# Kernel optimization log

Hardware: AMD Instinct MI355X
Metric: run time of the kernel (lower is better)

## Reference

```python
import jax, jax.numpy as jnp
import numpy as np

B, S, D = 4, 2048, 2048
D_INNER = max(128, D // 2)  # 1024, torch default d_inner
FO = 2                      # filter_order
K = 3                       # kernel_size
KS = 3                      # short_kernel_size


def setup_inputs() -> dict:
    key = jax.random.key(0)
    ks = jax.random.split(key, 6)
    return {
        "x": jax.random.normal(ks[0], (B, S, D), jnp.float32),
        # depthwise short conv: weight (D, KS), bias (D,)
        "short_w": jax.random.normal(ks[1], (D, KS), jnp.float32) / np.float32(np.sqrt(KS)),
        "short_b": jnp.zeros((D,), jnp.float32),
        # filter MLP proj: Linear(D -> FO*D_INNER)
        "proj_w": jax.random.normal(ks[2], (D, FO * D_INNER), jnp.float32) / np.float32(np.sqrt(D)),
        "proj_b": jnp.zeros((FO * D_INNER,), jnp.float32),
        # filter MLP output: Linear(D_INNER -> K), SHARED across filter orders
        "filt_w": jax.random.normal(ks[3], (D_INNER, K), jnp.float32) / np.float32(np.sqrt(D_INNER)),
        "filt_b": jnp.zeros((K,), jnp.float32),
        # output projection Linear(D -> D)
        "out_w": jax.random.normal(ks[4], (D, D), jnp.float32) / np.float32(np.sqrt(D)),
        "out_b": jnp.zeros((D,), jnp.float32),
    }


def reference(x, short_w, short_b, proj_w, proj_b, filt_w, filt_b, out_w, out_b):
    b, s, d = x.shape
    v = x  # v captured BEFORE short-conv residual, as in the torch code

    # --- causal depthwise short conv (pad k-1 on left, truncate to s) ---
    xp = jnp.pad(x, ((0, 0), (KS - 1, 0), (0, 0)))
    x_short = short_b
    for j in range(KS):  # tiny fixed kernel loop
        x_short = x_short + xp[:, j:j + s, :] * short_w[:, j]
    x = x + x_short

    # --- filter function: Linear -> GELU -> (shared) Linear -> tanh ---
    h = jax.nn.gelu(x @ proj_w + proj_b, approximate=False)         # (b, s, FO*D_INNER)
    h = h.reshape(b, s, FO, D_INNER)
    filt = jnp.tanh(jnp.einsum('bsfi,ik->bsfk', h, filt_w) + filt_b)  # (b, s, FO, K)

    # --- gated depthwise conv: kernel = mean over seq, shared across channels;
    # sum over filter orders commutes with the (linear) conv, so fold it in ---
    w = filt.mean(axis=1).sum(axis=1)                                # (b, K)
    xp2 = jnp.pad(x, ((0, 0), (K - 1, 0), (0, 0)))
    conv = jnp.zeros_like(x)
    for j in range(K):
        conv = conv + xp2[:, j:j + s, :] * w[:, j][:, None, None]

    # --- gate with v, GELU, output projection ---
    y = jax.nn.gelu(conv * v, approximate=False)
    return y @ out_w + out_b
```

## Files before the change

### kernel.cpp

```cpp
#include <hip/hip_runtime.h>
#include <hip/hip_bf16.h>
#include <math.h>

typedef unsigned short u16;
typedef __attribute__((ext_vector_type(4))) unsigned short u16x4;
typedef __attribute__((ext_vector_type(8))) unsigned short u16x8;
typedef __attribute__((ext_vector_type(8))) short s16x8;
typedef __attribute__((ext_vector_type(4))) float f32x4;

#define B_  4
#define S_  2048
#define D_  2048
#define DI_ 1024
#define MROWS (B_ * S_)
#define KDIM  D_
#define NDIM  D_
#define STRIP 16

__device__ __forceinline__ float b2f(u16 u) {
    union { unsigned i; float f; } v; v.i = ((unsigned)u) << 16; return v.f;
}
__device__ __forceinline__ u16 f2b(float f) {
    unsigned u = __float_as_uint(f);
    unsigned r = (u + 0x7FFFu + ((u >> 16) & 1u)) >> 16;
    return (u16)r;
}
__device__ __forceinline__ float gelu_exact(float x) {
    return 0.5f * x * (1.0f + erff(x * 0.70710678118654752f));
}

#define GLOAD_LDS16(gp, lp)                                                    \
    __builtin_amdgcn_global_load_lds(                                          \
        (const __attribute__((address_space(1))) void*)(gp),                   \
        (__attribute__((address_space(3))) void*)(lp), 16, 0, 0)

__global__ void prep_k(const float* __restrict__ in0, u16* __restrict__ out0,
                       const float* __restrict__ in1, u16* __restrict__ out1,
                       int nt,
                       const float* __restrict__ x, const float* __restrict__ sw,
                       const float* __restrict__ sb, u16* __restrict__ xs,
                       float* __restrict__ wacc, float* __restrict__ t_g,
                       unsigned* __restrict__ cnt) {
    const int bid = blockIdx.x;
    const int tid = threadIdx.x;
    const int tblocks = nt << 12;
    if (bid < tblocks) {
        __shared__ float tile[32][33];
        const float* in = (bid >> 12) ? in1 : in0;
        u16* out = (bid >> 12) ? out1 : out0;
        const int t2 = bid & 4095;
        const int bx = (t2 & 63) << 5, by = (t2 >> 6) << 5;
        const int tx = tid & 31, ty = tid >> 5;
        for (int i = 0; i < 32; i += 8)
            tile[ty + i][tx] = in[(size_t)(by + ty + i) * D_ + bx + tx];
        __syncthreads();
        for (int i = 0; i < 32; i += 8)
            out[(size_t)(bx + ty + i) * D_ + by + tx] = f2b(tile[tx][ty + i]);
        return;
    }
    const int f = bid - tblocks;
    {
        int z = f * 256 + tid;
        if (z < 12) wacc[z] = 0.0f;
        if (z == 12) *cnt = 0u;
        if (z < MROWS * 6) t_g[z] = 0.0f;
    }
    const int c = (f & 1) * 1024 + tid * 4;
    const int r0 = (f >> 1) * STRIP;
    const int t0 = r0 & (S_ - 1);

    float tap[12];
    #pragma unroll
    for (int q = 0; q < 3; ++q)
        ((f32x4*)tap)[q] = *(const f32x4*)(sw + (size_t)c * 3 + q * 4);
    f32x4 sbv = *(const f32x4*)(sb + c);

    const float* base = x + (size_t)r0 * D_ + c;
    f32x4 m2, m1;
    if (t0 == 0) { m2 = (f32x4)(0.0f); m1 = (f32x4)(0.0f); }
    else { m2 = *(const f32x4*)(base - 2 * D_); m1 = *(const f32x4*)(base - D_); }

    u16* op = xs + (size_t)r0 * D_ + c;
    #pragma unroll
    for (int rr = 0; rr < STRIP; ++rr) {
        f32x4 cur = *(const f32x4*)(base + (size_t)rr * D_);
        u16x4 outv;
        #pragma unroll
        for (int e = 0; e < 4; ++e) {
            float v = cur[e] + sbv[e]
                    + tap[e * 3 + 0] * m2[e]
                    + tap[e * 3 + 1] * m1[e]
                    + tap[e * 3 + 2] * cur[e];
            outv[e] = f2b(v);
        }
        *(u16x4*)(op + (size_t)rr * D_) = outv;
        m2 = m1; m1 = cur;
    }
}

__global__ void transpose_k(const float* __restrict__ in, u16* __restrict__ out) {
    __shared__ float tile[32][33];
    int bx = blockIdx.x * 32, by = blockIdx.y * 32;
    int tx = threadIdx.x & 31, ty = threadIdx.x >> 5;
    for (int i = 0; i < 32; i += 8)
        tile[ty + i][tx] = in[(size_t)(by + ty + i) * D_ + bx + tx];
    __syncthreads();
    for (int i = 0; i < 32; i += 8)
        out[(size_t)(bx + ty + i) * D_ + by + tx] = f2b(tile[tx][ty + i]);
}

#define STG_A(REG, KOFF) do { const u16* _g = gA + (KOFF);                     \
    GLOAD_LDS16(_g, &As[REG][ldsW0]);                                          \
    GLOAD_LDS16(_g + (size_t)128 * KDIM, &As[REG][ldsW1]); } while (0)
#define STG_B(REG, KOFF) do { const u16* _g = gB + (KOFF);                     \
    GLOAD_LDS16(_g, &Bs[REG][ldsW0]);                                          \
    GLOAD_LDS16(_g + (size_t)128 * KDIM, &Bs[REG][ldsW1]); } while (0)
#define LD_AH(R_) do {                                                         \
    aH[0] = *(const s16x8*)&As[R_][aoffR[4]];                                  \
    aH[1] = *(const s16x8*)&As[R_][aoffR[5]];                                  \
    aH[2] = *(const s16x8*)&As[R_][aoffR[6]];                                  \
    aH[3] = *(const s16x8*)&As[R_][aoffR[7]]; } while (0)
#define LD_ALBC(S_, R_) do {                                                   \
    aL[S_][0] = *(const s16x8*)&As[R_][aoffR[0]];                              \
    aL[S_][1] = *(const s16x8*)&As[R_][aoffR[1]];                              \
    aL[S_][2] = *(const s16x8*)&As[R_][aoffR[2]];                              \
    aL[S_][3] = *(const s16x8*)&As[R_][aoffR[3]];                              \
    bC[S_][0] = *(const s16x8*)&Bs[R_][boffR[0]];                              \
    bC[S_][1] = *(const s16x8*)&Bs[R_][boffR[1]];                              \
    bC[S_][2] = *(const s16x8*)&Bs[R_][boffR[2]];                              \
    bC[S_][3] = *(const s16x8*)&Bs[R_][boffR[3]]; } while (0)
#define MFMA_LO(S_) do { __builtin_amdgcn_s_setprio(1);                        \
    _Pragma("unroll")                                                          \
    for (int i_ = 0; i_ < 4; ++i_) {                                           \
        _Pragma("unroll")                                                      \
        for (int j_ = 0; j_ < 4; ++j_)                                         \
            acc[i_][j_] = __builtin_amdgcn_mfma_f32_16x16x32_bf16(             \
                aL[S_][i_], bC[S_][j_], acc[i_][j_], 0, 0, 0);                 \
    }                                                                          \
    __builtin_amdgcn_s_setprio(0); } while (0)
#define MFMA_HI(S_) do { __builtin_amdgcn_s_setprio(1);                        \
    _Pragma("unroll")                                                          \
    for (int i_ = 0; i_ < 4; ++i_) {                                           \
        _Pragma("unroll")                                                      \
        for (int j_ = 0; j_ < 4; ++j_)                                         \
            acc[4 + i_][j_] = __builtin_amdgcn_mfma_f32_16x16x32_bf16(         \
                aH[i_], bC[S_][j_], acc[4 + i_][j_], 0, 0, 0);                 \
    }                                                                          \
    __builtin_amdgcn_s_setprio(0); } while (0)
#define BARR() __builtin_amdgcn_s_barrier()
#define VM8() asm volatile("s_waitcnt vmcnt(8)" ::: "memory")
#define VM4() asm volatile("s_waitcnt vmcnt(4)" ::: "memory")
#define VM0() asm volatile("s_waitcnt vmcnt(0)" ::: "memory")
#define VMNOP()

#define TILE(T_, R_, RN_, CS_, NS_, DOSTG_, GATE_, DOPF_) do {                 \
    BARR();                                                                    \
    if (DOSTG_) { STG_A((((R_) + 3) & 3), ((T_) + 3) * 32);                    \
                  STG_B((((R_) + 3) & 3), ((T_) + 3) * 32); }                  \
    LD_AH(R_);                                                                 \
    MFMA_LO(CS_);                                                              \
    GATE_;                                                                     \
    BARR();                                                                    \
    if (DOPF_) { LD_ALBC(NS_, RN_); }                                          \
    MFMA_HI(CS_);                                                              \
} while (0)

#define GEMM_CORE_OL(APTR, BPTR)                                               \
    __shared__ u16 As[4][8192];                                                \
    __shared__ u16 Bs[4][8192];                                                \
    const int tid  = threadIdx.x;                                              \
    const int wid  = tid >> 6;                                                 \
    const int lane = tid & 63;                                                 \
    const int wr   = wid >> 2;                                                 \
    const int wc   = wid & 3;                                                  \
    const int lid_ = (blockIdx.y << 3) | blockIdx.x;                           \
    const int wsw_ = ((lid_ & 7) << 5) | (lid_ >> 3);         \
    const int row0 = (wsw_ >> 3) << 8;                                         \
    const int col0 = (wsw_ & 7) << 8;                                          \
    const int rowS    = tid >> 2;                                              \
    const int colOffS = (((tid & 3) ^ ((rowS >> 1) & 3)) << 3);                \
    const u16* gA = (APTR) + (size_t)(row0 + rowS) * KDIM + colOffS;           \
    const u16* gB = (BPTR) + (size_t)(col0 + rowS) * KDIM + colOffS;           \
    const int ldsW0 = wid * 512;                                               \
    const int ldsW1 = 4096 + wid * 512;                                        \
    int aoffR[8], boffR[4];                                                    \
    _Pragma("unroll")                                                          \
    for (int i = 0; i < 8; ++i) {                                              \
        int row  = (wr << 7) + (i << 4) + (lane & 15);                         \
        int slot = (lane >> 4) ^ ((row >> 1) & 3);                             \
        aoffR[i] = row * 32 + slot * 8;                                        \
    }                                                                          \
    _Pragma("unroll")                                                          \
    for (int j = 0; j < 4; ++j) {                                              \
        int row  = (wc << 6) + (j << 4) + (lane & 15);                         \
        int slot = (lane >> 4) ^ ((row >> 1) & 3);                             \
        boffR[j] = row * 32 + slot * 8;                                        \
    }                                                                          \
    f32x4 acc[8][4];                                                           \
    _Pragma("unroll")                                                          \
    for (int i = 0; i < 8; ++i)                                                \
        _Pragma("unroll")                                                      \
        for (int j = 0; j < 4; ++j) acc[i][j] = (f32x4)(0.0f);                 \
    s16x8 aL[2][4], bC[2][4], aH[4];                                           \
    STG_A(0, 0);  STG_B(0, 0);                                                 \
    STG_A(1, 32); STG_B(1, 32);                                                \
    STG_A(2, 64); STG_B(2, 64);                                                \
    VM8();                                                                     \
    BARR();                                                                    \
    LD_ALBC(0, 0);                                                             \
    _Pragma("unroll 1")                                                        \
    for (int t = 0; t < 15; ++t) {                                             \
        const int T4 = t * 4;                                                  \
        TILE(T4 + 0, 0, 1, 0, 1, 1, VM8(), 1);                                 \
        TILE(T4 + 1, 1, 2, 1, 0, 1, VM8(), 1);                                 \
        TILE(T4 + 2, 2, 3, 0, 1, 1, VM8(), 1);                                 \
        TILE(T4 + 3, 3, 0, 1, 0, 1, VM8(), 1);                                 \
    }                                                                          \
    TILE(60, 0, 1, 0, 1, 1, VM8(), 1);                                         \
    TILE(61, 1, 2, 1, 0, 0, VM4(), 1);                                         \
    TILE(62, 2, 3, 0, 1, 0, VM0(), 1);                                         \
    TILE(63, 3, 0, 1, 0, 0, VMNOP(), 0);

__global__ __launch_bounds__(512, 2)
void gemm_f8(const u16* __restrict__ A, const u16* __restrict__ BT,
             const float* __restrict__ bias,
             const float* __restrict__ fw, float* __restrict__ t_g,
             const float* __restrict__ fb, unsigned* __restrict__ cnt,
             float* __restrict__ wacc) {
    GEMM_CORE_OL(A, BT)

    __shared__ float t_lds[768];
    __shared__ unsigned done_s;
    __syncthreads();
    for (int z = tid; z < 768; z += 512) t_lds[z] = 0.0f;
    __syncthreads();

    const int colt0 = (wc << 6) + (lane & 15);
    float fwv[4][3], bsv[4];
    const int ibase = (col0 & (DI_ - 1)) + colt0;
    #pragma unroll
    for (int j = 0; j < 4; ++j) {
        int ifilt = ibase + j * 16;
        fwv[j][0] = fw[ifilt * 3 + 0];
        fwv[j][1] = fw[ifilt * 3 + 1];
        fwv[j][2] = fw[ifilt * 3 + 2];
        bsv[j] = bias[col0 + colt0 + j * 16];
    }
    #pragma unroll
    for (int i = 0; i < 8; ++i) {
        #pragma unroll
        for (int r = 0; r < 4; ++r) {
            float s0 = 0.f, s1 = 0.f, s2 = 0.f;
            #pragma unroll
            for (int j = 0; j < 4; ++j) {
                float hv = gelu_exact(acc[i][j][r] + bsv[j]);
                s0 += hv * fwv[j][0];
                s1 += hv * fwv[j][1];
                s2 += hv * fwv[j][2];
            }
            #pragma unroll
            for (int m = 1; m < 16; m <<= 1) {
                s0 += __shfl_xor(s0, m, 16);
                s1 += __shfl_xor(s1, m, 16);
                s2 += __shfl_xor(s2, m, 16);
            }
            if ((lane & 15) == 0) {
                int trow = (wr << 7) + ((lane >> 4) << 2) + (i << 4) + r;
                atomicAdd(&t_lds[trow * 3 + 0], s0);
                atomicAdd(&t_lds[trow * 3 + 1], s1);
                atomicAdd(&t_lds[trow * 3 + 2], s2);
            }
        }
    }
    __syncthreads();
    const int f3 = (col0 >= DI_) ? 3 : 0;
    for (int z = tid; z < 768; z += 512) {
        int rr = z / 3, k = z - rr * 3;
        atomicAdd(&t_g[(size_t)(row0 + rr) * 6 + f3 + k], t_lds[z]);
    }

    __threadfence();
    __syncthreads();
    if (tid == 0) done_s = atomicAdd(cnt, 1u);
    __syncthreads();
    if (done_s == 255u) {
        const float fb0 = fb[0], fb1 = fb[1], fb2 = fb[2];
        for (int b = 0; b < B_; ++b) {
            float s0 = 0.f, s1 = 0.f, s2 = 0.f;
            for (int p = tid; p < 2 * S_; p += 512) {
                int row = (b << 11) + (p >> 1);
                int fo  = p & 1;
                const float* tp = t_g + (size_t)row * 6 + fo * 3;
                float a0 = __hip_atomic_load(tp + 0, __ATOMIC_RELAXED,
                                             __HIP_MEMORY_SCOPE_AGENT);
                float a1 = __hip_atomic_load(tp + 1, __ATOMIC_RELAXED,
                                             __HIP_MEMORY_SCOPE_AGENT);
                float a2 = __hip_atomic_load(tp + 2, __ATOMIC_RELAXED,
                                             __HIP_MEMORY_SCOPE_AGENT);
                s0 += tanhf(a0 + fb0);
                s1 += tanhf(a1 + fb1);
                s2 += tanhf(a2 + fb2);
            }
            #pragma unroll
            for (int m = 1; m < 64; m <<= 1) {
                s0 += __shfl_xor(s0, m, 64);
                s1 += __shfl_xor(s1, m, 64);
                s2 += __shfl_xor(s2, m, 64);
            }
            __syncthreads();
            if (lane == 0) {
                t_lds[wid * 3 + 0] = s0;
                t_lds[wid * 3 + 1] = s1;
                t_lds[wid * 3 + 2] = s2;
            }
            __syncthreads();
            if (tid < 3) {
                float s = 0.f;
                #pragma unroll
                for (int w = 0; w < 8; ++w) s += t_lds[w * 3 + tid];
                wacc[b * 3 + tid] = s;
            }
        }
    }
}

__global__ __launch_bounds__(256, 2)
void gemm2_tlp(const u16* __restrict__ A, const u16* __restrict__ BT,
               const float* __restrict__ bias, float* __restrict__ C) {
    __shared__ u16 As[2][8192];
    __shared__ u16 Bs[2][4096];

    const int tid  = threadIdx.x;
    const int wid  = tid >> 6;
    const int lane = tid & 63;
    const int wr   = wid >> 1;
    const int wc   = wid & 1;
    const int lid  = (blockIdx.y << 4) | blockIdx.x;
    const int wsw  = ((lid & 7) << 6) | (lid >> 3);
    const int row0 = (wsw >> 4) << 8;
    const int col0 = (wsw & 15) << 7;

    const int srow = tid >> 2;
    const int cSw  = (((tid & 3) ^ ((srow >> 1) & 3)) << 3);
    const u16* gA0 = A  + (size_t)(row0 + srow) * KDIM + cSw;
    const u16* gB0 = BT + (size_t)(col0 + srow) * KDIM + cSw;
    const int ldsW = wid * 512;

#define STG2(R_, KOFF) do {                                                    \
    const u16* _ga = gA0 + (KOFF);                                             \
    const u16* _gb = gB0 + (KOFF);                                             \
    GLOAD_LDS16(_ga,                      &As[R_][ldsW]);                      \
    GLOAD_LDS16(_ga + (size_t)64 * KDIM,  &As[R_][2048 + ldsW]);               \
    GLOAD_LDS16(_ga + (size_t)128 * KDIM, &As[R_][4096 + ldsW]);               \
    GLOAD_LDS16(_ga + (size_t)192 * KDIM, &As[R_][6144 + ldsW]);               \
    GLOAD_LDS16(_gb,                      &Bs[R_][ldsW]);                      \
    GLOAD_LDS16(_gb + (size_t)64 * KDIM,  &Bs[R_][2048 + ldsW]);               \
} while (0)

    int aoffR[8], boffR[4];
    #pragma unroll
    for (int i = 0; i < 8; ++i) {
        int row  = (wr << 7) + (i << 4) + (lane & 15);
        int slot = (lane >> 4) ^ ((row >> 1) & 3);
        aoffR[i] = row * 32 + slot * 8;
    }
    #pragma unroll
    for (int j = 0; j < 4; ++j) {
        int row  = (wc << 6) + (j << 4) + (lane & 15);
        int slot = (lane >> 4) ^ ((row >> 1) & 3);
        boffR[j] = row * 32 + slot * 8;
    }

    f32x4 acc[8][4];
    #pragma unroll
    for (int i = 0; i < 8; ++i)
        #pragma unroll
        for (int j = 0; j < 4; ++j) acc[i][j] = (f32x4)(0.0f);

    STG2(0, 0);
    VM0();
    BARR();

    #pragma unroll 1
    for (int T = 0; T < 64; ++T) {
        const int cur = T & 1;
        if (T < 63) STG2(cur ^ 1, (T + 1) * 32);
        s16x8 af[8], bf[4];
        #pragma unroll
        for (int i = 0; i < 8; ++i) af[i] = *(const s16x8*)&As[cur][aoffR[i]];
        #pragma unroll
        for (int j = 0; j < 4; ++j) bf[j] = *(const s16x8*)&Bs[cur][boffR[j]];
        __builtin_amdgcn_s_setprio(1);
        #pragma unroll
        for (int i = 0; i < 8; ++i)
            #pragma unroll
            for (int j = 0; j < 4; ++j)
                acc[i][j] = __builtin_amdgcn_mfma_f32_16x16x32_bf16(
                    af[i], bf[j], acc[i][j], 0, 0, 0);
        __builtin_amdgcn_s_setprio(0);
        VM0();
        BARR();
    }
#undef STG2

    const int colt0 = (wc << 6) + (lane & 15);
    const int crow0 = row0 + (wr << 7) + ((lane >> 4) << 2);
    #pragma unroll
    for (int j = 0; j < 4; ++j) {
        int col = col0 + colt0 + j * 16;
        float bs = bias[col];
        #pragma unroll
        for (int i = 0; i < 8; ++i) {
            int rbase = crow0 + i * 16;
            #pragma unroll
            for (int r = 0; r < 4; ++r)
                C[(size_t)(rbase + r) * NDIM + col] = acc[i][j][r] + bs;
        }
    }
}

__global__ void gate_k(const u16* __restrict__ xs, const float* __restrict__ v,
                       const float* __restrict__ wacc, u16* __restrict__ g) {
    const int c = blockIdx.x * 1024 + threadIdx.x * 4;
    const int r0 = blockIdx.y * STRIP;
    const int t0 = r0 & (S_ - 1);
    const int b = r0 >> 11;
    const float w0 = wacc[b * 3 + 0] * (1.0f / (float)S_);
    const float w1 = wacc[b * 3 + 1] * (1.0f / (float)S_);
    const float w2 = wacc[b * 3 + 2] * (1.0f / (float)S_);

    const u16* base = xs + (size_t)r0 * D_ + c;
    f32x4 m2, m1;
    if (t0 == 0) {
        m2 = (f32x4)(0.0f); m1 = (f32x4)(0.0f);
    } else {
        u16x4 a2 = *(const u16x4*)(base - 2 * D_);
        u16x4 a1 = *(const u16x4*)(base - D_);
        #pragma unroll
        for (int e = 0; e < 4; ++e) { m2[e] = b2f(a2[e]); m1[e] = b2f(a1[e]); }
    }

    const float* vp = v + (size_t)r0 * D_ + c;
    u16* op = g + (size_t)r0 * D_ + c;
    #pragma unroll
    for (int rr = 0; rr < STRIP; ++rr) {
        u16x4 cb = *(const u16x4*)(base + (size_t)rr * D_);
        f32x4 vv = *(const f32x4*)(vp + (size_t)rr * D_);
        f32x4 cur;
        #pragma unroll
        for (int e = 0; e < 4; ++e) cur[e] = b2f(cb[e]);
        u16x4 outv;
        #pragma unroll
        for (int e = 0; e < 4; ++e) {
            float conv = w0 * m2[e] + w1 * m1[e] + w2 * cur[e];
            outv[e] = f2b(gelu_exact(conv * vv[e]));
        }
        *(u16x4*)(op + (size_t)rr * D_) = outv;
        m2 = m1; m1 = cur;
    }
}

extern "C" void kernel_launch(void* const* d_in, const int* in_sizes, int n_in,
                              void* d_out, int out_size, void* d_ws, size_t ws_size,
                              hipStream_t stream) {
    const float* x       = (const float*)d_in[0];
    const float* short_w = (const float*)d_in[1];
    const float* short_b = (const float*)d_in[2];
    const float* proj_w  = (const float*)d_in[3];
    const float* proj_b  = (const float*)d_in[4];
    const float* filt_w  = (const float*)d_in[5];
    const float* filt_b  = (const float*)d_in[6];
    const float* out_w   = (const float*)d_in[7];
    const float* out_b   = (const float*)d_in[8];
    float* out = (float*)d_out;

    char* ws = (char*)d_ws;
    const size_t xs_bytes = (size_t)MROWS * D_ * 2;
    const size_t wt_bytes = (size_t)KDIM * NDIM * 2;
    float*    wacc = (float*)(ws);
    unsigned* cnt  = (unsigned*)(ws + 512);
    float*    t_g  = (float*)(ws + 1024);
    u16*      xs   = (u16*)(ws + 262144);
    u16*      g    = (u16*)(ws + 262144 + xs_bytes);
    u16*      wT1  = (u16*)(ws + 262144 + 2 * xs_bytes);
    const size_t need_dual = 262144 + 2 * xs_bytes + 2 * wt_bytes;
    const bool dual = (ws_size >= need_dual);
    u16* wT2 = dual ? (u16*)(ws + 262144 + 2 * xs_bytes + wt_bytes) : wT1;

    if (dual) {
        prep_k<<<8192 + 1024, 256, 0, stream>>>(proj_w, wT1, out_w, wT2, 2,
                                                x, short_w, short_b, xs,
                                                wacc, t_g, cnt);
    } else {
        prep_k<<<4096 + 1024, 256, 0, stream>>>(proj_w, wT1, proj_w, wT1, 1,
                                                x, short_w, short_b, xs,
                                                wacc, t_g, cnt);
    }

    dim3 gg(NDIM / 256, MROWS / 256, 1);
    gemm_f8<<<gg, 512, 0, stream>>>(xs, wT1, proj_b, filt_w, t_g,
                                    filt_b, cnt, wacc);

    if (!dual) {
        dim3 tg(D_ / 32, D_ / 32, 1);
        transpose_k<<<tg, 256, 0, stream>>>(out_w, wT1);
    }

    dim3 cg(2, MROWS / STRIP, 1);
    gate_k<<<cg, 256, 0, stream>>>(xs, x, wacc, g);

    dim3 g2(NDIM / 128, MROWS / 256, 1);
    gemm2_tlp<<<g2, 256, 0, stream>>>(g, wT2, out_b, out);
}
```

Before: 402.0 us.

## Triple-buffer second GEMM and move filter reduction into separate kernel

New measurement: 359.4 us. 1.12x faster.

```diff
diff --git a/kernel.cpp b/kernel.cpp
--- a/kernel.cpp
+++ b/kernel.cpp
@@ -39,8 +39,7 @@
                        int nt,
                        const float* __restrict__ x, const float* __restrict__ sw,
                        const float* __restrict__ sb, u16* __restrict__ xs,
-                       float* __restrict__ wacc, float* __restrict__ t_g,
-                       unsigned* __restrict__ cnt) {
+                       float* __restrict__ wacc, float* __restrict__ t_g) {
     const int bid = blockIdx.x;
     const int tid = threadIdx.x;
     const int tblocks = nt << 12;
@@ -62,7 +61,6 @@
     {
         int z = f * 256 + tid;
         if (z < 12) wacc[z] = 0.0f;
-        if (z == 12) *cnt = 0u;
         if (z < MROWS * 6) t_g[z] = 0.0f;
     }
     const int c = (f & 1) * 1024 + tid * 4;
@@ -149,6 +147,7 @@
     __builtin_amdgcn_s_setprio(0); } while (0)
 #define BARR() __builtin_amdgcn_s_barrier()
 #define VM8() asm volatile("s_waitcnt vmcnt(8)" ::: "memory")
+#define VM6() asm volatile("s_waitcnt vmcnt(6)" ::: "memory")
 #define VM4() asm volatile("s_waitcnt vmcnt(4)" ::: "memory")
 #define VM0() asm volatile("s_waitcnt vmcnt(0)" ::: "memory")
 #define VMNOP()
@@ -224,13 +223,10 @@
 __global__ __launch_bounds__(512, 2)
 void gemm_f8(const u16* __restrict__ A, const u16* __restrict__ BT,
              const float* __restrict__ bias,
-             const float* __restrict__ fw, float* __restrict__ t_g,
-             const float* __restrict__ fb, unsigned* __restrict__ cnt,
-             float* __restrict__ wacc) {
+             const float* __restrict__ fw, float* __restrict__ t_g) {
     GEMM_CORE_OL(A, BT)
 
     __shared__ float t_lds[768];
-    __shared__ unsigned done_s;
     __syncthreads();
     for (int z = tid; z < 768; z += 512) t_lds[z] = 0.0f;
     __syncthreads();
@@ -278,57 +274,13 @@
         int rr = z / 3, k = z - rr * 3;
         atomicAdd(&t_g[(size_t)(row0 + rr) * 6 + f3 + k], t_lds[z]);
     }
-
-    __threadfence();
-    __syncthreads();
-    if (tid == 0) done_s = atomicAdd(cnt, 1u);
-    __syncthreads();
-    if (done_s == 255u) {
-        const float fb0 = fb[0], fb1 = fb[1], fb2 = fb[2];
-        for (int b = 0; b < B_; ++b) {
-            float s0 = 0.f, s1 = 0.f, s2 = 0.f;
-            for (int p = tid; p < 2 * S_; p += 512) {
-                int row = (b << 11) + (p >> 1);
-                int fo  = p & 1;
-                const float* tp = t_g + (size_t)row * 6 + fo * 3;
-                float a0 = __hip_atomic_load(tp + 0, __ATOMIC_RELAXED,
-                                             __HIP_MEMORY_SCOPE_AGENT);
-                float a1 = __hip_atomic_load(tp + 1, __ATOMIC_RELAXED,
-                                             __HIP_MEMORY_SCOPE_AGENT);
-                float a2 = __hip_atomic_load(tp + 2, __ATOMIC_RELAXED,
-                                             __HIP_MEMORY_SCOPE_AGENT);
-                s0 += tanhf(a0 + fb0);
-                s1 += tanhf(a1 + fb1);
-                s2 += tanhf(a2 + fb2);
-            }
-            #pragma unroll
-            for (int m = 1; m < 64; m <<= 1) {
-                s0 += __shfl_xor(s0, m, 64);
-                s1 += __shfl_xor(s1, m, 64);
-                s2 += __shfl_xor(s2, m, 64);
-            }
-            __syncthreads();
-            if (lane == 0) {
-                t_lds[wid * 3 + 0] = s0;
-                t_lds[wid * 3 + 1] = s1;
-                t_lds[wid * 3 + 2] = s2;
-            }
-            __syncthreads();
-            if (tid < 3) {
-                float s = 0.f;
-                #pragma unroll
-                for (int w = 0; w < 8; ++w) s += t_lds[w * 3 + tid];
-                wacc[b * 3 + tid] = s;
-            }
-        }
-    }
 }
 
 __global__ __launch_bounds__(256, 2)
 void gemm2_tlp(const u16* __restrict__ A, const u16* __restrict__ BT,
                const float* __restrict__ bias, float* __restrict__ C) {
-    __shared__ u16 As[2][8192];
-    __shared__ u16 Bs[2][4096];
+    __shared__ u16 As[3][8192];
+    __shared__ u16 Bs[3][4096];
 
     const int tid  = threadIdx.x;
     const int wid  = tid >> 6;
@@ -377,30 +329,55 @@
         #pragma unroll
         for (int j = 0; j < 4; ++j) acc[i][j] = (f32x4)(0.0f);
 
+#define MFMA_ALL() do { __builtin_amdgcn_s_setprio(1);                         \
+    _Pragma("unroll")                                                          \
+    for (int i_ = 0; i_ < 8; ++i_) {                                           \
+        _Pragma("unroll")                                                      \
+        for (int j_ = 0; j_ < 4; ++j_)                                         \
+            acc[i_][j_] = __builtin_amdgcn_mfma_f32_16x16x32_bf16(             \
+                af[i_], bf[j_], acc[i_][j_], 0, 0, 0);                         \
+    }                                                                          \
+    __builtin_amdgcn_s_setprio(0); } while (0)
+#define FRAGS(R_) do {                                                         \
+    _Pragma("unroll")                                                          \
+    for (int i_ = 0; i_ < 8; ++i_)                                             \
+        af[i_] = *(const s16x8*)&As[R_][aoffR[i_]];                            \
+    _Pragma("unroll")                                                          \
+    for (int j_ = 0; j_ < 4; ++j_)                                             \
+        bf[j_] = *(const s16x8*)&Bs[R_][boffR[j_]]; } while (0)
+
     STG2(0, 0);
-    VM0();
+    STG2(1, 32);
+    VM6();
     BARR();
 
+    int rc = 0, rs = 2;
     #pragma unroll 1
-    for (int T = 0; T < 64; ++T) {
-        const int cur = T & 1;
-        if (T < 63) STG2(cur ^ 1, (T + 1) * 32);
+    for (int T = 0; T < 62; ++T) {
+        STG2(rs, (T + 2) * 32);
         s16x8 af[8], bf[4];
-        #pragma unroll
-        for (int i = 0; i < 8; ++i) af[i] = *(const s16x8*)&As[cur][aoffR[i]];
-        #pragma unroll
-        for (int j = 0; j < 4; ++j) bf[j] = *(const s16x8*)&Bs[cur][boffR[j]];
-        __builtin_amdgcn_s_setprio(1);
-        #pragma unroll
-        for (int i = 0; i < 8; ++i)
-            #pragma unroll
-            for (int j = 0; j < 4; ++j)
-                acc[i][j] = __builtin_amdgcn_mfma_f32_16x16x32_bf16(
-                    af[i], bf[j], acc[i][j], 0, 0, 0);
-        __builtin_amdgcn_s_setprio(0);
+        FRAGS(rc);
+        MFMA_ALL();
+        VM6();
+        BARR();
+        rc = (rc == 2) ? 0 : rc + 1;
+        rs = (rs == 2) ? 0 : rs + 1;
+    }
+    {
+        s16x8 af[8], bf[4];
+        FRAGS(rc);
+        MFMA_ALL();
         VM0();
         BARR();
-    }
+        rc = (rc == 2) ? 0 : rc + 1;
+    }
+    {
+        s16x8 af[8], bf[4];
+        FRAGS(rc);
+        MFMA_ALL();
+    }
+#undef FRAGS
+#undef MFMA_ALL
 #undef STG2
 
     const int colt0 = (wc << 6) + (lane & 15);
@@ -416,6 +393,32 @@
             for (int r = 0; r < 4; ++r)
                 C[(size_t)(rbase + r) * NDIM + col] = acc[i][j][r] + bs;
         }
+    }
+}
+
+__global__ void filt_finish_k(const float* __restrict__ t_g, const float* __restrict__ fb,
+                              float* __restrict__ wacc) {
+    __shared__ float part[4][3];
+    const int tid = threadIdx.x;
+    int p = blockIdx.x * 256 + tid;
+    int row = p >> 1, f = p & 1;
+    const float* tp = t_g + (size_t)row * 6 + f * 3;
+    float v0 = tanhf(tp[0] + fb[0]);
+    float v1 = tanhf(tp[1] + fb[1]);
+    float v2 = tanhf(tp[2] + fb[2]);
+    #pragma unroll
+    for (int m = 1; m < 64; m <<= 1) {
+        v0 += __shfl_xor(v0, m, 64);
+        v1 += __shfl_xor(v1, m, 64);
+        v2 += __shfl_xor(v2, m, 64);
+    }
+    const int wid = tid >> 6, lane = tid & 63;
+    if (lane == 0) { part[wid][0] = v0; part[wid][1] = v1; part[wid][2] = v2; }
+    __syncthreads();
+    if (tid < 3) {
+        float s = part[0][tid] + part[1][tid] + part[2][tid] + part[3][tid];
+        int b = blockIdx.x >> 4;
+        atomicAdd(&wacc[b * 3 + tid], s);
     }
 }
 
@@ -478,7 +481,6 @@
     const size_t xs_bytes = (size_t)MROWS * D_ * 2;
     const size_t wt_bytes = (size_t)KDIM * NDIM * 2;
     float*    wacc = (float*)(ws);
-    unsigned* cnt  = (unsigned*)(ws + 512);
     float*    t_g  = (float*)(ws + 1024);
     u16*      xs   = (u16*)(ws + 262144);
     u16*      g    = (u16*)(ws + 262144 + xs_bytes);
@@ -490,16 +492,17 @@
     if (dual) {
         prep_k<<<8192 + 1024, 256, 0, stream>>>(proj_w, wT1, out_w, wT2, 2,
                                                 x, short_w, short_b, xs,
-                                                wacc, t_g, cnt);
+                                                wacc, t_g);
     } else {
         prep_k<<<4096 + 1024, 256, 0, stream>>>(proj_w, wT1, proj_w, wT1, 1,
                                                 x, short_w, short_b, xs,
-                                                wacc, t_g, cnt);
+                                                wacc, t_g);
     }
 
     dim3 gg(NDIM / 256, MROWS / 256, 1);
-    gemm_f8<<<gg, 512, 0, stream>>>(xs, wT1, proj_b, filt_w, t_g,
-                                    filt_b, cnt, wacc);
+    gemm_f8<<<gg, 512, 0, stream>>>(xs, wT1, proj_b, filt_w, t_g);
+
+    filt_finish_k<<<64, 256, 0, stream>>>(t_g, filt_b, wacc);
 
     if (!dual) {
         dim3 tg(D_ / 32, D_ / 32, 1);
```
